# Kernel tuning notes

Hardware: AMD Instinct MI355X
Metric: run time of the kernel (lower is better)

The kernel has to match this reference:

```python
import jax, jax.numpy as jnp
import numpy as np

N_NODES = 20000
N_EDGES = 640000
D = 128          # vision_dim == topo_dim
OUT = 256        # out_dim
B = 64           # image batch == num graphs
HW = 64
NEG_SLOPE = 0.2


def _sn(w2d, u):
    """PyTorch spectral_norm forward: one power iteration (u,v detached), W/sigma."""
    v = jax.lax.stop_gradient(w2d.T @ u)
    v = v / (jnp.linalg.norm(v) + 1e-12)
    u2 = jax.lax.stop_gradient(w2d @ v)
    u2 = u2 / (jnp.linalg.norm(u2) + 1e-12)
    sigma = u2 @ (w2d @ v)
    return w2d / sigma


def _leaky(x):
    return jnp.where(x >= 0, x, NEG_SLOPE * x)


def setup_inputs() -> dict:
    key = jax.random.key(0)
    ks = jax.random.split(key, 16)
    vis = jax.random.normal(ks[0], (B, D, HW, HW), dtype=jnp.float32)
    topo = jax.random.normal(ks[1], (N_NODES, D), dtype=jnp.float32)
    edge_index = jax.random.randint(ks[2], (2, N_EDGES), 0, N_NODES, dtype=jnp.int64)
    batch = jnp.sort(jax.random.randint(ks[3], (N_NODES,), 0, B, dtype=jnp.int64))
    s = 0.05
    conv_w = jax.random.normal(ks[4], (D, D, 3, 3), dtype=jnp.float32) * s
    conv_b = jnp.zeros((D,), dtype=jnp.float32)
    conv_u = jax.random.normal(ks[5], (D,), dtype=jnp.float32)
    fcv_w = jax.random.normal(ks[6], (OUT, D * 4), dtype=jnp.float32) * s
    fcv_b = jnp.zeros((OUT,), dtype=jnp.float32)
    fcv_u = jax.random.normal(ks[7], (OUT,), dtype=jnp.float32)
    gcn_w = jax.random.normal(ks[8], (D, D), dtype=jnp.float32) * s
    gcn_b = jnp.zeros((D,), dtype=jnp.float32)
    fct_w = jax.random.normal(ks[9], (OUT, D), dtype=jnp.float32) * s
    fct_b = jnp.zeros((OUT,), dtype=jnp.float32)
    fct_u = jax.random.normal(ks[10], (OUT,), dtype=jnp.float32)
    return dict(vis=vis, topo=topo, edge_index=edge_index, batch=batch,
                conv_w=conv_w, conv_b=conv_b, conv_u=conv_u,
                fcv_w=fcv_w, fcv_b=fcv_b, fcv_u=fcv_u,
                gcn_w=gcn_w, gcn_b=gcn_b,
                fct_w=fct_w, fct_b=fct_b, fct_u=fct_u)


def reference(vis, topo, edge_index, batch,
              conv_w, conv_b, conv_u,
              fcv_w, fcv_b, fcv_u,
              gcn_w, gcn_b,
              fct_w, fct_b, fct_u):
    # ---- vision head: spectral-norm conv3x3 -> leaky_relu -> adaptive max pool 2x2 -> SN linear
    cw = _sn(conv_w.reshape(D, -1), conv_u).reshape(conv_w.shape)
    x = jax.lax.conv_general_dilated(vis, cw, window_strides=(1, 1), padding='VALID',
                                     dimension_numbers=('NCHW', 'OIHW', 'NCHW'))
    x = _leaky(x + conv_b[None, :, None, None])              # [B, D, 62, 62]
    Bc, C, H, W = x.shape
    x = x.reshape(Bc, C, 2, H // 2, 2, W // 2).max(axis=(3, 5))  # adaptive max pool -> [B,D,2,2]
    x = x.reshape(Bc, -1)                                    # [B, 4D]
    vis_score = x @ _sn(fcv_w, fcv_u).T + fcv_b              # [B, OUT]

    # ---- topo head: GCNConv (sym-norm, self-loops) -> leaky_relu -> global max pool -> SN linear
    n = topo.shape[0]
    loop = jnp.arange(n, dtype=edge_index.dtype)
    src = jnp.concatenate([edge_index[0], loop])
    dst = jnp.concatenate([edge_index[1], loop])
    deg = jax.ops.segment_sum(jnp.ones_like(dst, dtype=topo.dtype), dst, num_segments=n)
    dis = jnp.where(deg > 0, jax.lax.rsqrt(jnp.maximum(deg, 1.0)), 0.0)
    norm = dis[src] * dis[dst]                               # [E+N]
    xw = topo @ gcn_w                                        # [N, D]
    h = jax.ops.segment_sum(norm[:, None] * xw[src], dst, num_segments=n) + gcn_b
    h = _leaky(h)
    pooled = jax.ops.segment_max(h, batch, num_segments=B)   # [B, D]
    topo_score = pooled @ _sn(fct_w, fct_u).T + fct_b        # [B, OUT]

    return (vis_score, topo_score)
```

## Files before the change

kernel.cpp:

```cpp
#include <hip/hip_runtime.h>
#include <hip/hip_bf16.h>
#include <float.h>
#include <stdint.h>

#define NB   64
#define CD   128
#define OUTD 256
#define NNODE 20000
#define NEDGE 640000

typedef __bf16 bf16x8 __attribute__((ext_vector_type(8)));
typedef __bf16 bf16x4 __attribute__((ext_vector_type(4)));
typedef float  f32x4  __attribute__((ext_vector_type(4)));

__device__ inline void gl_lds16(const void* g, void* l) {
  __builtin_amdgcn_global_load_lds(
      (const __attribute__((address_space(1))) void*)g,
      (__attribute__((address_space(3))) void*)l, 16, 0, 0);
}

__device__ inline void atomicMaxF(float* addr, float val) {
  if (val >= 0.f) atomicMax((int*)addr, __float_as_int(val));
  else            atomicMin((unsigned int*)addr, __float_as_uint(val));
}

__global__ void k_init(float* __restrict__ pooled_v, float* __restrict__ pooled_t,
                       int* __restrict__ cnt, int* __restrict__ fill,
                       float* __restrict__ sn_scratch, int* __restrict__ ntotal) {
  const int i = blockIdx.x * 256 + threadIdx.x;
  if (i < NB * CD * 4) pooled_v[i] = -FLT_MAX;
  if (i < NB * CD)     pooled_t[i] = -FLT_MAX;
  if (i < NNODE)       { cnt[i] = 0; fill[i] = 0; }
  if (i < 1796)        sn_scratch[i] = 0.0f;
  if (i == 0)          *ntotal = 0;
}

__global__ __launch_bounds__(256) void k_sn_v(const float* __restrict__ conv_w, const float* __restrict__ conv_u,
                                              const float* __restrict__ fcv_w,  const float* __restrict__ fcv_u,
                                              const float* __restrict__ fct_w,  const float* __restrict__ fct_u,
                                              float* __restrict__ sn) {
  const int bb = blockIdx.x;
  const float* W; const float* u; float* v; int C; int r0;
  if (bb < 16)      { W = conv_w; u = conv_u; v = sn;        C = 1152; r0 = bb * 8; }
  else if (bb < 48) { W = fcv_w;  u = fcv_u;  v = sn + 1152; C = 512;  r0 = (bb - 16) * 8; }
  else              { W = fct_w;  u = fct_u;  v = sn + 1664; C = 128;  r0 = (bb - 48) * 8; }
  const int tid = threadIdx.x;
  float acc[5] = {0.f, 0.f, 0.f, 0.f, 0.f};
  for (int i = r0; i < r0 + 8; ++i) {
    const float ui = u[i];
    const float* row = W + (size_t)i * C;
    #pragma unroll
    for (int t = 0; t < 5; ++t) {
      const int j = tid + t * 256;
      if (j < C) acc[t] += ui * row[j];
    }
  }
  #pragma unroll
  for (int t = 0; t < 5; ++t) {
    const int j = tid + t * 256;
    if (j < C) atomicAdd(&v[j], acc[t]);
  }
}

__global__ __launch_bounds__(256) void k_sn_w(const float* __restrict__ conv_w,
                                              const float* __restrict__ fcv_w,
                                              const float* __restrict__ fct_w,
                                              float* __restrict__ sn) {
  const int gw = blockIdx.x * 4 + (threadIdx.x >> 6);
  const int lane = threadIdx.x & 63;
  const float* W; const float* v; int C, m, row;
  if (gw < 128)      { W = conv_w; v = sn;        C = 1152; m = 0; row = gw; }
  else if (gw < 384) { W = fcv_w;  v = sn + 1152; C = 512;  m = 1; row = gw - 128; }
  else               { W = fct_w;  v = sn + 1664; C = 128;  m = 2; row = gw - 384; }
  const float* wr = W + (size_t)row * C;
  float y = 0.f;
  for (int c = lane; c < C; c += 64) y += wr[c] * v[c];
  #pragma unroll
  for (int s = 32; s > 0; s >>= 1) y += __shfl_xor(y, s, 64);
  if (lane == 0) atomicAdd(&sn[1792 + m], y * y);
}

__global__ __launch_bounds__(256) void k_sn_fin(const float* __restrict__ sn, float* __restrict__ inv_sigma) {
  __shared__ float red[256];
  const int tid = threadIdx.x;
  const int off[4] = {0, 1152, 1664, 1792};
  for (int m = 0; m < 3; ++m) {
    const int C = off[m + 1] - off[m];
    float ss = 0.f;
    for (int j = tid; j < C; j += 256) { const float a = sn[off[m] + j]; ss += a * a; }
    red[tid] = ss; __syncthreads();
    for (int s = 128; s > 0; s >>= 1) { if (tid < s) red[tid] += red[tid + s]; __syncthreads(); }
    if (tid == 0) inv_sigma[m] = (sqrtf(red[0]) + 1e-12f) / sqrtf(sn[1792 + m]);
    __syncthreads();
  }
}

__global__ __launch_bounds__(256) void k_prep(const float* __restrict__ vis, __hip_bfloat16* __restrict__ visT2,
                                              const float* __restrict__ conv_w, const float* __restrict__ inv_sigma,
                                              __hip_bfloat16* __restrict__ Bt2,
                                              const int* __restrict__ dst, int* __restrict__ cnt) {
  __shared__ float tile[8192];
  const int bid = blockIdx.x;
  const int t = threadIdx.x;
  if (bid < 4096) {
    const int b = bid >> 6, y = bid & 63;
    const int c0 = t >> 4, x4 = (t & 15) << 2;
    const float* src = vis + (size_t)b * 524288 + y * 64;
    #pragma unroll
    for (int i = 0; i < 8; ++i) {
      const int c = i * 16 + c0;
      *(f32x4*)&tile[c * 64 + x4] = *(const f32x4*)(src + (size_t)c * 4096 + x4);
    }
    __syncthreads();
    bf16x8* dstv = (bf16x8*)(visT2 + ((size_t)bid << 13));
    #pragma unroll
    for (int k = 0; k < 4; ++k) {
      const int j = k * 256 + t;
      const int g = j >> 6, x = j & 63;
      union { bf16x8 v; __hip_bfloat16 h[8]; } u;
      #pragma unroll
      for (int cc = 0; cc < 8; ++cc)
        u.h[cc] = __float2bfloat16(tile[(g * 8 + cc) * 64 + x]);
      dstv[j] = u.v;
    }
  } else if (bid < 4672) {
    const int tt = (bid - 4096) * 256 + t;
    if (tt < 147456) {
      const int j = tt & 7, n = (tt >> 3) & 127, s = (tt >> 10) & 7, hk = (tt >> 13) & 1, tap = tt >> 14;
      const int ci = hk * 64 + s * 8 + j;
      Bt2[tt] = __float2bfloat16(conv_w[n * 1152 + ci * 9 + tap] * inv_sigma[0]);
    }
  } else {
    const int e = (bid - 4672) * 256 + t;
    if (e < NEDGE) atomicAdd(&cnt[dst[e]], 1);
  }
}

__global__ __launch_bounds__(256, 4) void k_conv(const __hip_bfloat16* __restrict__ visT2,
                                                 const __hip_bfloat16* __restrict__ Bt2,
                                                 const float* __restrict__ conv_b,
                                                 float* __restrict__ pooled_v, int b0) {
  __shared__ bf16x8 lds_a[1024];
  __shared__ bf16x8 lds_b[1024];
  const int bx = blockIdx.x;
  const int b = b0 + bx / 31;
  const int y0 = (bx % 31) * 2;
  const int tid = threadIdx.x;
  const int wave = tid >> 6, lane = tid & 63;
  const int quad = lane >> 4, l15 = lane & 15;

  f32x4 acc[8][2];
  #pragma unroll
  for (int i = 0; i < 8; ++i) {
    acc[i][0] = f32x4{0.f, 0.f, 0.f, 0.f};
    acc[i][1] = f32x4{0.f, 0.f, 0.f, 0.f};
  }

  const __hip_bfloat16* vb = visT2 + ((size_t)b << 19);
  const int s0 = wave << 1;
  bf16x8* ldsA0 = &lds_a[s0 << 7];
  bf16x8* ldsB0 = &lds_b[s0 << 7];
  const int lane8 = lane << 3;

  for (int ky = 0; ky < 3; ++ky) {
    for (int kx = 0; kx < 3; ++kx) {
      const int tap = ky * 3 + kx;
      #pragma unroll
      for (int hk = 0; hk < 2; ++hk) {
        const __hip_bfloat16* a0p = vb + ((size_t)(((y0 + ky) << 4) + (hk << 3) + s0) << 9) + (kx << 3) + lane8;
        const __hip_bfloat16* a1p = vb + ((size_t)(((y0 + 1 + ky) << 4) + (hk << 3) + s0) << 9) + (kx << 3) + lane8;
        const __hip_bfloat16* bp  = Bt2 + (((size_t)(((tap << 1) + hk) << 3) + s0) << 10) + lane8;
        gl_lds16(a0p,        ldsA0);
        gl_lds16(a1p,        ldsA0 + 64);
        gl_lds16(a0p + 512,  ldsA0 + 128);
        gl_lds16(a1p + 512,  ldsA0 + 192);
        gl_lds16(bp,         ldsB0);
        gl_lds16(bp + 512,   ldsB0 + 64);
        gl_lds16(bp + 1024,  ldsB0 + 128);
        gl_lds16(bp + 1536,  ldsB0 + 192);
        __syncthreads();
        const bf16x8 b00 = lds_b[(quad << 7) + (wave << 5) + l15];
        const bf16x8 b01 = lds_b[(quad << 7) + (wave << 5) + 16 + l15];
        const bf16x8 b10 = lds_b[((4 + quad) << 7) + (wave << 5) + l15];
        const bf16x8 b11 = lds_b[((4 + quad) << 7) + (wave << 5) + 16 + l15];
        #pragma unroll
        for (int mt = 0; mt < 8; ++mt) {
          const bf16x8 a0 = lds_a[(quad << 7) + (mt << 4) + l15];
          const bf16x8 a1 = lds_a[((4 + quad) << 7) + (mt << 4) + l15];
          acc[mt][0] = __builtin_amdgcn_mfma_f32_16x16x32_bf16(a0, b00, acc[mt][0], 0, 0, 0);
          acc[mt][1] = __builtin_amdgcn_mfma_f32_16x16x32_bf16(a0, b01, acc[mt][1], 0, 0, 0);
          acc[mt][0] = __builtin_amdgcn_mfma_f32_16x16x32_bf16(a1, b10, acc[mt][0], 0, 0, 0);
          acc[mt][1] = __builtin_amdgcn_mfma_f32_16x16x32_bf16(a1, b11, acc[mt][1], 0, 0, 0);
        }
        __syncthreads();
      }
    }
  }

  const float cb0 = conv_b[(wave << 5) + l15];
  const float cb1 = conv_b[(wave << 5) + 16 + l15];
  float pmax[2][2][2];
  #pragma unroll
  for (int i = 0; i < 8; ++i) (&pmax[0][0][0])[i] = -FLT_MAX;

  #pragma unroll
  for (int mt = 0; mt < 8; ++mt) {
    const int py = (y0 + (mt >> 2)) >= 31 ? 1 : 0;
    #pragma unroll
    for (int r = 0; r < 4; ++r) {
      const int x = ((mt & 3) << 4) + (quad << 2) + r;
      if (x < 62) {
        const int px = x >= 31 ? 1 : 0;
        float v0 = acc[mt][0][r] + cb0;  v0 = v0 >= 0.f ? v0 : 0.2f * v0;
        float v1 = acc[mt][1][r] + cb1;  v1 = v1 >= 0.f ? v1 : 0.2f * v1;
        pmax[0][py][px] = fmaxf(pmax[0][py][px], v0);
        pmax[1][py][px] = fmaxf(pmax[1][py][px], v1);
      }
    }
  }
  #pragma unroll
  for (int nt = 0; nt < 2; ++nt)
    #pragma unroll
    for (int py = 0; py < 2; ++py)
      #pragma unroll
      for (int px = 0; px < 2; ++px) {
        float v = pmax[nt][py][px];
        v = fmaxf(v, __shfl_xor(v, 16, 64));
        v = fmaxf(v, __shfl_xor(v, 32, 64));
        if (quad == 0) {
          const int n = (wave << 5) + (nt << 4) + l15;
          atomicMaxF(&pooled_v[(size_t)b * 512 + n * 4 + py * 2 + px], v);
        }
      }
}

__global__ __launch_bounds__(256) void k_scan_xw(const int* __restrict__ cnt, int* __restrict__ offset,
                                                 int* __restrict__ total, float* __restrict__ dis,
                                                 const float* __restrict__ topo, const float* __restrict__ gcn_w,
                                                 __bf16* __restrict__ xws) {
  __shared__ f32x4 w4[4096];
  __shared__ int sbase;
  const int tid = threadIdx.x;
  if (blockIdx.x < 79) {
    int* red = (int*)w4;
    const int n = blockIdx.x * 256 + tid;
    const int v = (n < NNODE) ? cnt[n] : 0;
    red[tid] = v; __syncthreads();
    for (int d = 1; d < 256; d <<= 1) {
      const int t = (tid >= d) ? red[tid - d] : 0;
      __syncthreads();
      red[tid] += t;
      __syncthreads();
    }
    if (tid == 255) sbase = atomicAdd(total, red[255]);
    __syncthreads();
    if (n < NNODE) {
      offset[n] = sbase + red[tid] - v;
      dis[n] = rsqrtf((float)(v + 1));
    }
  } else {
    const f32x4* gw4 = (const f32x4*)gcn_w;
    for (int i = tid; i < 4096; i += 256) w4[i] = gw4[i];
    __syncthreads();
    const int n0 = (blockIdx.x - 79) * 64;
    const int jq = tid & 31, ns = tid >> 5;
    for (int pass = 0; pass < 8; ++pass) {
      const int n = n0 + pass * 8 + ns;
      if (n >= NNODE) break;
      const f32x4* tr4 = (const f32x4*)(topo + (size_t)n * 128);
      f32x4 a = {0.f, 0.f, 0.f, 0.f};
      for (int d4 = 0; d4 < 32; ++d4) {
        const f32x4 t = tr4[d4];
        const int base = (d4 << 7) + jq;
        #pragma unroll
        for (int m = 0; m < 4; ++m) {
          const f32x4 w = w4[base + m * 32];
          #pragma unroll
          for (int k = 0; k < 4; ++k) a[k] += t[m] * w[k];
        }
      }
      const float dn = rsqrtf((float)(cnt[n] + 1));
      bf16x4 o;
      #pragma unroll
      for (int k = 0; k < 4; ++k) o[k] = (__bf16)(a[k] * dn);
      ((bf16x4*)xws)[(size_t)n * 32 + jq] = o;
    }
  }
}

__global__ void k_bucket(const int* __restrict__ src, const int* __restrict__ dst,
                         const int* __restrict__ offset, int* __restrict__ fill,
                         int* __restrict__ sorted_src) {
  const int e = blockIdx.x * 256 + threadIdx.x;
  if (e >= NEDGE) return;
  const int t = dst[e];
  const int pos = atomicAdd(&fill[t], 1);
  sorted_src[offset[t] + pos] = src[e];
}

__global__ __launch_bounds__(256) void k_gather(const int* __restrict__ sorted_src,
                                                const int* __restrict__ offset, const int* __restrict__ cnt,
                                                const float* __restrict__ dis, const __bf16* __restrict__ xws,
                                                const float* __restrict__ gcn_b, const int* __restrict__ batch,
                                                float* __restrict__ pooled_t) {
  __shared__ float hred[4][128];
  __shared__ int hg[4];
  const int wave = threadIdx.x >> 6, lane = threadIdx.x & 63;
  const int n = blockIdx.x * 4 + wave;
  const int slot = lane >> 4, l16 = lane & 15;
  const int e0 = offset[n], ne = cnt[n];
  const bf16x8* x8 = (const bf16x8*)xws;
  float a[8];
  if (slot == 0) {
    const bf16x8 v = x8[(size_t)n * 16 + l16];
    #pragma unroll
    for (int k = 0; k < 8; ++k) a[k] = (float)v[k];
  } else {
    #pragma unroll
    for (int k = 0; k < 8; ++k) a[k] = 0.f;
  }
  for (int e = slot; e < ne; e += 4) {
    const int s = sorted_src[e0 + e];
    const bf16x8 v = x8[(size_t)s * 16 + l16];
    #pragma unroll
    for (int k = 0; k < 8; ++k) a[k] += (float)v[k];
  }
  #pragma unroll
  for (int k = 0; k < 8; ++k) {
    a[k] += __shfl_xor(a[k], 16, 64);
    a[k] += __shfl_xor(a[k], 32, 64);
  }
  if (lane == 0) hg[wave] = batch[n];
  if (slot == 0) {
    const float dn = dis[n];
    #pragma unroll
    for (int k = 0; k < 8; ++k) {
      float t = gcn_b[(l16 << 3) + k] + dn * a[k];
      hred[wave][(l16 << 3) + k] = t >= 0.f ? t : 0.2f * t;
    }
  }
  __syncthreads();
  const int tid = threadIdx.x;
  if (tid < 128) {
    const int g0 = hg[0], g1 = hg[1], g2 = hg[2], g3 = hg[3];
    if (g0 == g1 && g1 == g2 && g2 == g3) {
      const float m = fmaxf(fmaxf(hred[0][tid], hred[1][tid]), fmaxf(hred[2][tid], hred[3][tid]));
      atomicMaxF(&pooled_t[g0 * 128 + tid], m);
    } else {
      atomicMaxF(&pooled_t[g0 * 128 + tid], hred[0][tid]);
      atomicMaxF(&pooled_t[g1 * 128 + tid], hred[1][tid]);
      atomicMaxF(&pooled_t[g2 * 128 + tid], hred[2][tid]);
      atomicMaxF(&pooled_t[g3 * 128 + tid], hred[3][tid]);
    }
  }
}

__global__ __launch_bounds__(256) void k_fc(const float* __restrict__ pooled_v, const float* __restrict__ fcv_w,
                                            const float* __restrict__ fcv_b,
                                            const float* __restrict__ pooled_t, const float* __restrict__ fct_w,
                                            const float* __restrict__ fct_b,
                                            const float* __restrict__ inv_sigma, float* __restrict__ out) {
  const int tid = threadIdx.x;
  if (blockIdx.x < 64) {
    __shared__ f32x4 xr[128];
    const int b = blockIdx.x;
    if (tid < 128) xr[tid] = ((const f32x4*)pooled_v)[b * 128 + tid];
    __syncthreads();
    const f32x4* wr = (const f32x4*)(fcv_w + (size_t)tid * 512);
    f32x4 a4 = {0.f, 0.f, 0.f, 0.f};
    for (int f = 0; f < 128; ++f) {
      const f32x4 x = xr[f];
      const f32x4 w = wr[f];
      #pragma unroll
      for (int k = 0; k < 4; ++k) a4[k] += x[k] * w[k];
    }
    const float a = a4[0] + a4[1] + a4[2] + a4[3];
    out[b * 256 + tid] = a * inv_sigma[1] + fcv_b[tid];
  } else {
    __shared__ f32x4 xr2[32];
    const int b = blockIdx.x - 64;
    if (tid < 32) xr2[tid] = ((const f32x4*)pooled_t)[b * 32 + tid];
    __syncthreads();
    const f32x4* wr = (const f32x4*)(fct_w + (size_t)tid * 128);
    f32x4 a4 = {0.f, 0.f, 0.f, 0.f};
    for (int f = 0; f < 32; ++f) {
      const f32x4 x = xr2[f];
      const f32x4 w = wr[f];
      #pragma unroll
      for (int k = 0; k < 4; ++k) a4[k] += x[k] * w[k];
    }
    const float a = a4[0] + a4[1] + a4[2] + a4[3];
    out[NB * 256 + b * 256 + tid] = a * inv_sigma[2] + fct_b[tid];
  }
}

extern "C" void kernel_launch(void* const* d_in, const int* in_sizes, int n_in,
                              void* d_out, int out_size, void* d_ws, size_t ws_size,
                              hipStream_t stream) {
  const float* vis    = (const float*)d_in[0];
  const float* topo   = (const float*)d_in[1];
  const int*   eidx   = (const int*)d_in[2];
  const int*   batch  = (const int*)d_in[3];
  const float* conv_w = (const float*)d_in[4];
  const float* conv_b = (const float*)d_in[5];
  const float* conv_u = (const float*)d_in[6];
  const float* fcv_w  = (const float*)d_in[7];
  const float* fcv_b  = (const float*)d_in[8];
  const float* fcv_u  = (const float*)d_in[9];
  const float* gcn_w  = (const float*)d_in[10];
  const float* gcn_b  = (const float*)d_in[11];
  const float* fct_w  = (const float*)d_in[12];
  const float* fct_b  = (const float*)d_in[13];
  const float* fct_u  = (const float*)d_in[14];
  float* out = (float*)d_out;

  char* p = (char*)d_ws;
  float* inv_sigma  = (float*)p; p += 256;
  float* sn_scratch = (float*)p; p += 1796 * 4 + 240;
  float* pooled_v   = (float*)p; p += (size_t)NB * 512 * 4;
  float* pooled_t   = (float*)p; p += (size_t)NB * 128 * 4;
  int*   cnt        = (int*)p;   p += (size_t)NNODE * 4;
  int*   offset     = (int*)p;   p += (size_t)NNODE * 4;
  int*   fill       = (int*)p;   p += (size_t)NNODE * 4;
  float* dis        = (float*)p; p += (size_t)NNODE * 4;
  int*   ntotal     = (int*)p;   p += 256;
  int*   sorted_src = (int*)p;   p += (size_t)NEDGE * 4;
  __bf16* xws       = (__bf16*)p; p += (size_t)NNODE * 128 * 2 + 256;
  __hip_bfloat16* Bt2 = (__hip_bfloat16*)p; p += (size_t)147456 * 2;
  p = (char*)(((uintptr_t)p + 255) & ~(uintptr_t)255);
  __hip_bfloat16* visT2 = (__hip_bfloat16*)p;

  hipLaunchKernelGGL(k_init,    dim3(128),  dim3(256), 0, stream, pooled_v, pooled_t, cnt, fill, sn_scratch, ntotal);
  hipLaunchKernelGGL(k_sn_v,    dim3(80),   dim3(256), 0, stream, conv_w, conv_u, fcv_w, fcv_u, fct_w, fct_u, sn_scratch);
  hipLaunchKernelGGL(k_sn_w,    dim3(160),  dim3(256), 0, stream, conv_w, fcv_w, fct_w, sn_scratch);
  hipLaunchKernelGGL(k_sn_fin,  dim3(1),    dim3(256), 0, stream, sn_scratch, inv_sigma);
  hipLaunchKernelGGL(k_prep,    dim3(7172), dim3(256), 0, stream, vis, visT2, conv_w, inv_sigma, Bt2, eidx + NEDGE, cnt);
  hipLaunchKernelGGL(k_conv,    dim3(32*31), dim3(256), 0, stream, visT2, Bt2, conv_b, pooled_v, 0);
  hipLaunchKernelGGL(k_conv,    dim3(32*31), dim3(256), 0, stream, visT2, Bt2, conv_b, pooled_v, 32);
  hipLaunchKernelGGL(k_scan_xw, dim3(392),  dim3(256), 0, stream, cnt, offset, ntotal, dis, topo, gcn_w, xws);
  hipLaunchKernelGGL(k_bucket,  dim3(2500), dim3(256), 0, stream, eidx, eidx + NEDGE, offset, fill, sorted_src);
  hipLaunchKernelGGL(k_gather,  dim3(5000), dim3(256), 0, stream, sorted_src, offset, cnt, dis, xws, gcn_b, batch, pooled_t);
  hipLaunchKernelGGL(k_fc,      dim3(128),  dim3(256), 0, stream, pooled_v, fcv_w, fcv_b, pooled_t, fct_w, fct_b, inv_sigma, out);
}
```

Before: 487.2 us.

## Fuse edge bucketing into conv kernel and enlarge vis transpose tiles

After: 475.7 us. 1.02x faster.

```diff
diff --git a/kernel.cpp b/kernel.cpp
--- a/kernel.cpp
+++ b/kernel.cpp
@@ -95,55 +95,75 @@
   }
 }
 
-__global__ __launch_bounds__(256) void k_prep(const float* __restrict__ vis, __hip_bfloat16* __restrict__ visT2,
-                                              const float* __restrict__ conv_w, const float* __restrict__ inv_sigma,
-                                              __hip_bfloat16* __restrict__ Bt2,
-                                              const int* __restrict__ dst, int* __restrict__ cnt) {
-  __shared__ float tile[8192];
+__global__ __launch_bounds__(256, 2) void k_prep(const float* __restrict__ vis, __bf16* __restrict__ visT2,
+                                                 const float* __restrict__ conv_w, const float* __restrict__ inv_sigma,
+                                                 __hip_bfloat16* __restrict__ Bt2,
+                                                 const int* __restrict__ dst, int* __restrict__ cnt) {
+  __shared__ __bf16 tile[32768];
   const int bid = blockIdx.x;
   const int t = threadIdx.x;
-  if (bid < 4096) {
-    const int b = bid >> 6, y = bid & 63;
-    const int c0 = t >> 4, x4 = (t & 15) << 2;
-    const float* src = vis + (size_t)b * 524288 + y * 64;
-    #pragma unroll
-    for (int i = 0; i < 8; ++i) {
-      const int c = i * 16 + c0;
-      *(f32x4*)&tile[c * 64 + x4] = *(const f32x4*)(src + (size_t)c * 4096 + x4);
-    }
-    __syncthreads();
-    bf16x8* dstv = (bf16x8*)(visT2 + ((size_t)bid << 13));
-    #pragma unroll
-    for (int k = 0; k < 4; ++k) {
-      const int j = k * 256 + t;
-      const int g = j >> 6, x = j & 63;
-      union { bf16x8 v; __hip_bfloat16 h[8]; } u;
-      #pragma unroll
-      for (int cc = 0; cc < 8; ++cc)
-        u.h[cc] = __float2bfloat16(tile[(g * 8 + cc) * 64 + x]);
-      dstv[j] = u.v;
-    }
-  } else if (bid < 4672) {
-    const int tt = (bid - 4096) * 256 + t;
+  if (bid < 1024) {
+    const int b = bid >> 4, y0 = (bid & 15) << 2;
+    const int wave = t >> 6, lane = t & 63;
+    const float* src = vis + (size_t)b * 524288 + y0 * 64 + lane * 4;
+    #pragma unroll
+    for (int i = 0; i < 32; ++i) {
+      const int c = wave * 32 + i;
+      const f32x4 v = *(const f32x4*)(src + (size_t)c * 4096);
+      bf16x4 o;
+      #pragma unroll
+      for (int k = 0; k < 4; ++k) o[k] = (__bf16)v[k];
+      *(bf16x4*)&tile[c * 256 + lane * 4] = o;
+    }
+    __syncthreads();
+    #pragma unroll
+    for (int yy = 0; yy < 4; ++yy) {
+      bf16x8* dstv = (bf16x8*)(visT2 + ((size_t)((b << 6) + y0 + yy) << 13));
+      #pragma unroll
+      for (int k = 0; k < 4; ++k) {
+        const int j = k * 256 + t;
+        const int g = j >> 6, x = j & 63;
+        union { bf16x8 v; __bf16 h[8]; } u;
+        #pragma unroll
+        for (int cc = 0; cc < 8; ++cc)
+          u.h[cc] = tile[(g * 8 + cc) * 256 + yy * 64 + x];
+        dstv[j] = u.v;
+      }
+    }
+  } else if (bid < 1600) {
+    const int tt = (bid - 1024) * 256 + t;
     if (tt < 147456) {
       const int j = tt & 7, n = (tt >> 3) & 127, s = (tt >> 10) & 7, hk = (tt >> 13) & 1, tap = tt >> 14;
       const int ci = hk * 64 + s * 8 + j;
       Bt2[tt] = __float2bfloat16(conv_w[n * 1152 + ci * 9 + tap] * inv_sigma[0]);
     }
   } else {
-    const int e = (bid - 4672) * 256 + t;
+    const int e = (bid - 1600) * 256 + t;
     if (e < NEDGE) atomicAdd(&cnt[dst[e]], 1);
   }
 }
 
-__global__ __launch_bounds__(256, 4) void k_conv(const __hip_bfloat16* __restrict__ visT2,
-                                                 const __hip_bfloat16* __restrict__ Bt2,
-                                                 const float* __restrict__ conv_b,
-                                                 float* __restrict__ pooled_v, int b0) {
+__global__ __launch_bounds__(256, 4) void k_convb(const __hip_bfloat16* __restrict__ visT2,
+                                                  const __hip_bfloat16* __restrict__ Bt2,
+                                                  const float* __restrict__ conv_b,
+                                                  float* __restrict__ pooled_v,
+                                                  const int* __restrict__ srcE, const int* __restrict__ dstE,
+                                                  const int* __restrict__ offset, int* __restrict__ fill,
+                                                  int* __restrict__ sorted_src) {
   __shared__ bf16x8 lds_a[1024];
   __shared__ bf16x8 lds_b[1024];
-  const int bx = blockIdx.x;
-  const int b = b0 + bx / 31;
+  const int bid = blockIdx.x;
+  if (bid >= 1984) {
+    const int e = (bid - 1984) * 256 + threadIdx.x;
+    if (e < NEDGE) {
+      const int tt = dstE[e];
+      const int pos = atomicAdd(&fill[tt], 1);
+      sorted_src[offset[tt] + pos] = srcE[e];
+    }
+    return;
+  }
+  const int bx = bid;
+  const int b = bx / 31;
   const int y0 = (bx % 31) * 2;
   const int tid = threadIdx.x;
   const int wave = tid >> 6, lane = tid & 63;
@@ -288,16 +308,6 @@
   }
 }
 
-__global__ void k_bucket(const int* __restrict__ src, const int* __restrict__ dst,
-                         const int* __restrict__ offset, int* __restrict__ fill,
-                         int* __restrict__ sorted_src) {
-  const int e = blockIdx.x * 256 + threadIdx.x;
-  if (e >= NEDGE) return;
-  const int t = dst[e];
-  const int pos = atomicAdd(&fill[t], 1);
-  sorted_src[offset[t] + pos] = src[e];
-}
-
 __global__ __launch_bounds__(256) void k_gather(const int* __restrict__ sorted_src,
                                                 const int* __restrict__ offset, const int* __restrict__ cnt,
                                                 const float* __restrict__ dis, const __bf16* __restrict__ xws,
@@ -428,17 +438,16 @@
   __bf16* xws       = (__bf16*)p; p += (size_t)NNODE * 128 * 2 + 256;
   __hip_bfloat16* Bt2 = (__hip_bfloat16*)p; p += (size_t)147456 * 2;
   p = (char*)(((uintptr_t)p + 255) & ~(uintptr_t)255);
-  __hip_bfloat16* visT2 = (__hip_bfloat16*)p;
+  __bf16* visT2 = (__bf16*)p;
 
   hipLaunchKernelGGL(k_init,    dim3(128),  dim3(256), 0, stream, pooled_v, pooled_t, cnt, fill, sn_scratch, ntotal);
   hipLaunchKernelGGL(k_sn_v,    dim3(80),   dim3(256), 0, stream, conv_w, conv_u, fcv_w, fcv_u, fct_w, fct_u, sn_scratch);
   hipLaunchKernelGGL(k_sn_w,    dim3(160),  dim3(256), 0, stream, conv_w, fcv_w, fct_w, sn_scratch);
   hipLaunchKernelGGL(k_sn_fin,  dim3(1),    dim3(256), 0, stream, sn_scratch, inv_sigma);
-  hipLaunchKernelGGL(k_prep,    dim3(7172), dim3(256), 0, stream, vis, visT2, conv_w, inv_sigma, Bt2, eidx + NEDGE, cnt);
-  hipLaunchKernelGGL(k_conv,    dim3(32*31), dim3(256), 0, stream, visT2, Bt2, conv_b, pooled_v, 0);
-  hipLaunchKernelGGL(k_conv,    dim3(32*31), dim3(256), 0, stream, visT2, Bt2, conv_b, pooled_v, 32);
+  hipLaunchKernelGGL(k_prep,    dim3(4100), dim3(256), 0, stream, vis, visT2, conv_w, inv_sigma, Bt2, eidx + NEDGE, cnt);
   hipLaunchKernelGGL(k_scan_xw, dim3(392),  dim3(256), 0, stream, cnt, offset, ntotal, dis, topo, gcn_w, xws);
-  hipLaunchKernelGGL(k_bucket,  dim3(2500), dim3(256), 0, stream, eidx, eidx + NEDGE, offset, fill, sorted_src);
+  hipLaunchKernelGGL(k_convb,   dim3(4484), dim3(256), 0, stream, (const __hip_bfloat16*)visT2, Bt2, conv_b, pooled_v,
+                     eidx, eidx + NEDGE, offset, fill, sorted_src);
   hipLaunchKernelGGL(k_gather,  dim3(5000), dim3(256), 0, stream, sorted_src, offset, cnt, dis, xws, gcn_b, batch, pooled_t);
   hipLaunchKernelGGL(k_fc,      dim3(128),  dim3(256), 0, stream, pooled_v, fcv_w, fcv_b, pooled_t, fct_w, fct_b, inv_sigma, out);
 }
```
